# Performance work log

Measured on AMD Instinct MI355X. Metric: run time of the kernel, lower is better.

Reference implementation:

```python
import jax, jax.numpy as jnp
import numpy as np

N = 50000      # nodes
E = 800000     # edges (before self loops)
F_IN = 128     # dataset.num_features
HID = 32       # hidden_channels (per GAT head)
HEADS = 4
C = 40         # dataset.num_classes
NEG_SLOPE = 0.2


def setup_inputs() -> dict:
    key = jax.random.key(0)
    ks = jax.random.split(key, 18)
    g = lambda k, shape, fan: jax.random.normal(k, shape, dtype=jnp.float32) / np.sqrt(fan)
    inp = {
        "x": jax.random.normal(ks[0], (N, F_IN), dtype=jnp.float32),
        "edge_index": jax.random.randint(ks[1], (2, E), 0, N, dtype=jnp.int64),
        # GAT layer 1: F_IN -> HEADS*HID
        "gat_W1": g(ks[2], (F_IN, HEADS * HID), F_IN),
        "gat_att_src1": g(ks[3], (HEADS, HID), HID),
        "gat_att_dst1": g(ks[4], (HEADS, HID), HID),
        "gat_b1": jnp.zeros((HEADS * HID,), jnp.float32),
        # GAT layer 2: HEADS*HID -> C, heads=1
        "gat_W2": g(ks[5], (HEADS * HID, C), HEADS * HID),
        "gat_att_src2": g(ks[6], (1, C), C),
        "gat_att_dst2": g(ks[7], (1, C), C),
        "gat_b2": jnp.zeros((C,), jnp.float32),
        # GCN layers
        "gcn_W1": g(ks[8], (F_IN, HID), F_IN),
        "gcn_b1": jnp.zeros((HID,), jnp.float32),
        "gcn_W2": g(ks[9], (HID, C), HID),
        "gcn_b2": jnp.zeros((C,), jnp.float32),
        # final linear: 2C -> C
        "lin_W": g(ks[10], (2 * C, C), 2 * C),
        "lin_b": jnp.zeros((C,), jnp.float32),
        "weight_c": jnp.float32(0.5),
        "weight_t": jnp.float32(0.5),
    }
    return inp


def _add_self_loops(src, dst, n):
    loop = jnp.arange(n, dtype=src.dtype)
    return jnp.concatenate([src, loop]), jnp.concatenate([dst, loop])


def _gat_conv(x, src, dst, n, W, att_src, att_dst, b, heads, out_dim):
    # h: [n, heads, out_dim]
    h = (x @ W).reshape(n, heads, out_dim)
    a_s = jnp.einsum('nhd,hd->nh', h, att_src)   # source-side attention logit
    a_d = jnp.einsum('nhd,hd->nh', h, att_dst)   # target-side attention logit
    e = jax.nn.leaky_relu(a_s[src] + a_d[dst], NEG_SLOPE)  # [E', heads]
    # softmax over incoming edges of each target node (self loops guarantee >=1 edge)
    m = jax.ops.segment_max(e, dst, num_segments=n)
    ex = jnp.exp(e - m[dst])
    s = jax.ops.segment_sum(ex, dst, num_segments=n)
    alpha = ex / s[dst]                          # [E', heads]
    out = jax.ops.segment_sum(h[src] * alpha[..., None], dst, num_segments=n)
    return out.reshape(n, heads * out_dim) + b


def _gcn_conv(x, src, dst, n, W, b):
    h = x @ W
    deg = jax.ops.segment_sum(jnp.ones(src.shape, h.dtype), dst, num_segments=n)
    norm = jax.lax.rsqrt(deg)                    # deg >= 1 (self loops)
    coef = (norm[src] * norm[dst])[:, None]
    return jax.ops.segment_sum(h[src] * coef, dst, num_segments=n) + b


def reference(x, edge_index, gat_W1, gat_att_src1, gat_att_dst1, gat_b1,
              gat_W2, gat_att_src2, gat_att_dst2, gat_b2,
              gcn_W1, gcn_b1, gcn_W2, gcn_b2, lin_W, lin_b,
              weight_c, weight_t):
    n = x.shape[0]
    src, dst = _add_self_loops(edge_index[0], edge_index[1], n)
    # GAT branch (dropout is identity at inference)
    x_gat = _gat_conv(x, src, dst, n, gat_W1, gat_att_src1, gat_att_dst1,
                      gat_b1, HEADS, HID)
    x_gat = jax.nn.elu(x_gat)
    x_gat = _gat_conv(x_gat, src, dst, n, gat_W2, gat_att_src2, gat_att_dst2,
                      gat_b2, 1, C)
    # GCN branch
    x_gcn = jax.nn.relu(_gcn_conv(x, src, dst, n, gcn_W1, gcn_b1))
    x_gcn = _gcn_conv(x_gcn, src, dst, n, gcn_W2, gcn_b2)
    # weighted feature concat + linear head
    cat = jnp.concatenate([x_gcn * weight_c, x_gat * weight_t], axis=1)  # [n, 2C]
    return cat @ lin_W + lin_b
```

## Files before the change

### kernel.cpp

```cpp
#include <hip/hip_runtime.h>
#include <math.h>

#define F_IN   128
#define HIDC   32
#define NHEAD  4
#define CDIM   40
#define NEG_SLOPE 0.2f
#define BCAP   4096
#define OVCAP  16384
#define SCHUNK 4096

typedef __attribute__((ext_vector_type(8))) short bf16x8;
typedef __attribute__((ext_vector_type(4))) float f32x4;

__device__ __forceinline__ float leakyf(float x) { return x > 0.f ? x : NEG_SLOPE * x; }

__device__ __forceinline__ float sel4(float4 v, int h) {
    return (h == 0) ? v.x : (h == 1) ? v.y : (h == 2) ? v.z : v.w;
}
__device__ __forceinline__ unsigned pack2_bf16(float a, float b) {
    unsigned ua = __float_as_uint(a);
    unsigned ub = __float_as_uint(b);
    ua = (ua + 0x7FFFu + ((ua >> 16) & 1u)) >> 16;
    ub = (ub + 0x7FFFu + ((ub >> 16) & 1u)) >> 16;
    return ua | (ub << 16);
}
__device__ __forceinline__ float2 unpack2_bf16(unsigned p) {
    return make_float2(__uint_as_float(p << 16), __uint_as_float(p & 0xFFFF0000u));
}

__global__ void wb_prep_kernel(const float* __restrict__ Wg, const float* __restrict__ Wc,
                               uint4* __restrict__ wbf)
{
    int b = blockIdx.x;
    int lane = threadIdx.x;
    int nt = b >> 2, ks = b & 3;
    int c = nt * 16 + (lane & 15);
    int k0 = ks * 32 + (lane >> 4) * 8;
    unsigned u[4];
#pragma unroll
    for (int jj = 0; jj < 4; ++jj) {
        int k = k0 + 2 * jj;
        float a0 = (c < 128) ? Wg[(size_t)k * 128 + c] : Wc[(size_t)k * 32 + (c - 128)];
        float a1 = (c < 128) ? Wg[(size_t)(k + 1) * 128 + c] : Wc[(size_t)(k + 1) * 32 + (c - 128)];
        u[jj] = pack2_bf16(a0, a1);
    }
    wbf[(size_t)b * 64 + lane] = make_uint4(u[0], u[1], u[2], u[3]);
}

__global__ __launch_bounds__(256) void gemm1_mfma_kernel(
    const float* __restrict__ X, const uint4* __restrict__ wbf,
    const float* __restrict__ aw_s, const float* __restrict__ aw_d,
    unsigned* __restrict__ hb,
    float* __restrict__ as1, float* __restrict__ ad1, int n)
{
    __shared__ float Ct[64][164];
    __shared__ float sw[128], dw[128];
    const int tid = threadIdx.x;
    const int w = tid >> 6, lane = tid & 63;
    const int m = lane & 15, q = lane >> 4;
    const int node0 = blockIdx.x * 64;
    if (tid < 128) { sw[tid] = aw_s[tid]; dw[tid] = aw_d[tid]; }

    f32x4 acc[10];
#pragma unroll
    for (int t = 0; t < 10; ++t) acc[t] = (f32x4){0.f, 0.f, 0.f, 0.f};

    const int row = node0 + w * 16 + m;
    const bool rv = row < n;
#pragma unroll
    for (int ks = 0; ks < 4; ++ks) {
        uint4 pa = make_uint4(0u, 0u, 0u, 0u);
        if (rv) {
            const float* xr = X + (size_t)row * 128 + ks * 32 + q * 8;
            float4 a0 = *(const float4*)xr;
            float4 a1 = *(const float4*)(xr + 4);
            pa = make_uint4(pack2_bf16(a0.x, a0.y), pack2_bf16(a0.z, a0.w),
                            pack2_bf16(a1.x, a1.y), pack2_bf16(a1.z, a1.w));
        }
        bf16x8 af = *(bf16x8*)&pa;
#pragma unroll
        for (int nt = 0; nt < 10; ++nt) {
            uint4 pb = wbf[(size_t)(nt * 4 + ks) * 64 + lane];
            bf16x8 bfv = *(bf16x8*)&pb;
            acc[nt] = __builtin_amdgcn_mfma_f32_16x16x32_bf16(af, bfv, acc[nt], 0, 0, 0);
        }
    }
#pragma unroll
    for (int nt = 0; nt < 10; ++nt)
#pragma unroll
        for (int r = 0; r < 4; ++r)
            Ct[w * 16 + q * 4 + r][nt * 16 + m] = acc[nt][r];
    __syncthreads();

    for (int i = tid; i < 64 * 64; i += 256) {
        int nd = i >> 6, u = i & 63;
        int gn = node0 + nd;
        if (gn < n)
            hb[(size_t)gn * 80 + u] = pack2_bf16(Ct[nd][2 * u], Ct[nd][2 * u + 1]);
    }
    for (int i = tid; i < 64 * 16; i += 256) {
        int nd = i >> 4, u = i & 15;
        int gn = node0 + nd;
        if (gn < n)
            hb[(size_t)gn * 80 + 64 + u] = pack2_bf16(Ct[nd][128 + 2 * u], Ct[nd][128 + 2 * u + 1]);
    }
    {
        int nd = tid >> 2, h = tid & 3;
        int gn = node0 + nd;
        if (gn < n) {
            float s = 0.f, d = 0.f;
#pragma unroll
            for (int k = 0; k < HIDC; ++k) {
                float v = Ct[nd][h * HIDC + k];
                s = fmaf(v, sw[h * HIDC + k], s);
                d = fmaf(v, dw[h * HIDC + k], d);
            }
            as1[(size_t)gn * 4 + h] = s;
            ad1[(size_t)gn * 4 + h] = d;
        }
    }
}

template<int K, int OUTC, int BN, int BK, int OSTRIDE = OUTC>
__global__ __launch_bounds__((OUTC / 4) * (BN / 4)) void gemm_tile(
    const float* __restrict__ X, const float* __restrict__ W,
    const float* __restrict__ bias, float* __restrict__ Y, int n)
{
    constexpr int CG = OUTC / 4;
    constexpr int NG = BN / 4;
    constexpr int NT = CG * NG;
    __shared__ float Xs[BK][BN + 4];
    __shared__ float Ws[BK][OUTC];
    const int tid = threadIdx.x;
    const int cg = tid % CG, ng = tid / CG;
    const int node0 = blockIdx.x * BN;
    float acc[4][4] = {};

    for (int kb = 0; kb < K; kb += BK) {
        for (int idx = tid; idx < BN * (BK / 4); idx += NT) {
            int nd = idx / (BK / 4);
            int kq = idx % (BK / 4);
            int gnode = node0 + nd;
            float4 v = (gnode < n) ? *(const float4*)&X[(size_t)gnode * K + kb + kq * 4]
                                   : make_float4(0.f, 0.f, 0.f, 0.f);
            Xs[kq * 4 + 0][nd] = v.x;
            Xs[kq * 4 + 1][nd] = v.y;
            Xs[kq * 4 + 2][nd] = v.z;
            Xs[kq * 4 + 3][nd] = v.w;
        }
        for (int idx = tid; idx < BK * CG; idx += NT) {
            int kk = idx / CG;
            int cq = idx % CG;
            *(float4*)&Ws[kk][cq * 4] = *(const float4*)&W[(size_t)(kb + kk) * OUTC + cq * 4];
        }
        __syncthreads();
#pragma unroll
        for (int k = 0; k < BK; ++k) {
            float4 xv = *(const float4*)&Xs[k][ng * 4];
            float4 wv = *(const float4*)&Ws[k][cg * 4];
            float xa[4] = {xv.x, xv.y, xv.z, xv.w};
            float wa[4] = {wv.x, wv.y, wv.z, wv.w};
#pragma unroll
            for (int j = 0; j < 4; ++j)
#pragma unroll
                for (int c = 0; c < 4; ++c)
                    acc[j][c] = fmaf(xa[j], wa[c], acc[j][c]);
        }
        __syncthreads();
    }

    float4 bv = make_float4(0.f, 0.f, 0.f, 0.f);
    if (bias) bv = *(const float4*)&bias[cg * 4];
#pragma unroll
    for (int j = 0; j < 4; ++j) {
        int gnode = node0 + ng * 4 + j;
        if (gnode < n) {
            float4 o = make_float4(acc[j][0] + bv.x, acc[j][1] + bv.y,
                                   acc[j][2] + bv.z, acc[j][3] + bv.w);
            *(float4*)&Y[(size_t)gnode * OSTRIDE + cg * 4] = o;
        }
    }
}

template<int K, int OUTC, int BN, int BK, int OSTRIDE_U, int OFF_U>
__global__ __launch_bounds__((OUTC / 4) * (BN / 4)) void gemm_tile_bb(
    const unsigned* __restrict__ Xb, const float* __restrict__ W,
    unsigned* __restrict__ Yb, int n)
{
    constexpr int CG = OUTC / 4;
    constexpr int NG = BN / 4;
    constexpr int NT = CG * NG;
    __shared__ float Xs[BK][BN + 4];
    __shared__ float Ws[BK][OUTC];
    const int tid = threadIdx.x;
    const int cg = tid % CG, ng = tid / CG;
    const int node0 = blockIdx.x * BN;
    float acc[4][4] = {};

    for (int kb = 0; kb < K; kb += BK) {
        for (int idx = tid; idx < BN * (BK / 8); idx += NT) {
            int nd = idx / (BK / 8);
            int kq = idx % (BK / 8);
            int gnode = node0 + nd;
            uint4 v = (gnode < n) ? *(const uint4*)&Xb[(size_t)gnode * (K / 2) + kb / 2 + kq * 4]
                                  : make_uint4(0u, 0u, 0u, 0u);
            float2 a = unpack2_bf16(v.x), b = unpack2_bf16(v.y);
            float2 c = unpack2_bf16(v.z), d = unpack2_bf16(v.w);
            Xs[kq * 8 + 0][nd] = a.x; Xs[kq * 8 + 1][nd] = a.y;
            Xs[kq * 8 + 2][nd] = b.x; Xs[kq * 8 + 3][nd] = b.y;
            Xs[kq * 8 + 4][nd] = c.x; Xs[kq * 8 + 5][nd] = c.y;
            Xs[kq * 8 + 6][nd] = d.x; Xs[kq * 8 + 7][nd] = d.y;
        }
        for (int idx = tid; idx < BK * CG; idx += NT) {
            int kk = idx / CG;
            int cq = idx % CG;
            *(float4*)&Ws[kk][cq * 4] = *(const float4*)&W[(size_t)(kb + kk) * OUTC + cq * 4];
        }
        __syncthreads();
#pragma unroll
        for (int k = 0; k < BK; ++k) {
            float4 xv = *(const float4*)&Xs[k][ng * 4];
            float4 wv = *(const float4*)&Ws[k][cg * 4];
            float xa[4] = {xv.x, xv.y, xv.z, xv.w};
            float wa[4] = {wv.x, wv.y, wv.z, wv.w};
#pragma unroll
            for (int j = 0; j < 4; ++j)
#pragma unroll
                for (int c = 0; c < 4; ++c)
                    acc[j][c] = fmaf(xa[j], wa[c], acc[j][c]);
        }
        __syncthreads();
    }

#pragma unroll
    for (int j = 0; j < 4; ++j) {
        int gnode = node0 + ng * 4 + j;
        if (gnode < n) {
            uint2 pb = make_uint2(pack2_bf16(acc[j][0], acc[j][1]),
                                  pack2_bf16(acc[j][2], acc[j][3]));
            *(uint2*)&Yb[(size_t)gnode * OSTRIDE_U + OFF_U + cg * 2] = pb;
        }
    }
}

__global__ __launch_bounds__(320) void gemm2_gat_kernel(
    const unsigned* __restrict__ Xb, const float* __restrict__ W,
    const float* __restrict__ aw_s, const float* __restrict__ aw_d,
    unsigned* __restrict__ Yb, float* __restrict__ as2, float* __restrict__ ad2, int n)
{
    constexpr int K = 128, OUTC = 40, BN = 128, BK = 32;
    constexpr int CG = OUTC / 4, NT = 320;
    __shared__ float smem[32 * 132 + 32 * 40];
    float* Xs = smem;
    float* Ws = smem + 32 * 132;
    const int tid = threadIdx.x;
    const int cg = tid % CG, ng = tid / CG;
    const int node0 = blockIdx.x * BN;
    float acc[4][4] = {};

    for (int kb = 0; kb < K; kb += BK) {
        for (int idx = tid; idx < BN * (BK / 8); idx += NT) {
            int nd = idx / (BK / 8);
            int kq = idx % (BK / 8);
            int gnode = node0 + nd;
            uint4 v = (gnode < n) ? *(const uint4*)&Xb[(size_t)gnode * (K / 2) + kb / 2 + kq * 4]
                                  : make_uint4(0u, 0u, 0u, 0u);
            float2 a = unpack2_bf16(v.x), b = unpack2_bf16(v.y);
            float2 c = unpack2_bf16(v.z), d = unpack2_bf16(v.w);
            Xs[(kq * 8 + 0) * 132 + nd] = a.x; Xs[(kq * 8 + 1) * 132 + nd] = a.y;
            Xs[(kq * 8 + 2) * 132 + nd] = b.x; Xs[(kq * 8 + 3) * 132 + nd] = b.y;
            Xs[(kq * 8 + 4) * 132 + nd] = c.x; Xs[(kq * 8 + 5) * 132 + nd] = c.y;
            Xs[(kq * 8 + 6) * 132 + nd] = d.x; Xs[(kq * 8 + 7) * 132 + nd] = d.y;
        }
        for (int idx = tid; idx < BK * CG; idx += NT) {
            int kk = idx / CG;
            int cq = idx % CG;
            *(float4*)&Ws[kk * 40 + cq * 4] = *(const float4*)&W[(size_t)(kb + kk) * OUTC + cq * 4];
        }
        __syncthreads();
#pragma unroll
        for (int k = 0; k < BK; ++k) {
            float4 xv = *(const float4*)&Xs[k * 132 + ng * 4];
            float4 wv = *(const float4*)&Ws[k * 40 + cg * 4];
            float xa[4] = {xv.x, xv.y, xv.z, xv.w};
            float wa[4] = {wv.x, wv.y, wv.z, wv.w};
#pragma unroll
            for (int j = 0; j < 4; ++j)
#pragma unroll
                for (int c = 0; c < 4; ++c)
                    acc[j][c] = fmaf(xa[j], wa[c], acc[j][c]);
        }
        __syncthreads();
    }

    float* Ct  = smem;
    float* sww = smem + 128 * 41;
    float* dww = sww + 40;
#pragma unroll
    for (int j = 0; j < 4; ++j) {
        int gnode = node0 + ng * 4 + j;
        if (gnode < n) {
            uint2 pb = make_uint2(pack2_bf16(acc[j][0], acc[j][1]),
                                  pack2_bf16(acc[j][2], acc[j][3]));
            *(uint2*)&Yb[(size_t)gnode * 40 + cg * 2] = pb;
        }
#pragma unroll
        for (int c = 0; c < 4; ++c)
            Ct[(ng * 4 + j) * 41 + cg * 4 + c] = acc[j][c];
    }
    if (tid < 40) { sww[tid] = aw_s[tid]; dww[tid] = aw_d[tid]; }
    __syncthreads();
    if (tid < 128) {
        int gnode = node0 + tid;
        if (gnode < n) {
            float s = 0.f, d = 0.f;
#pragma unroll
            for (int c = 0; c < 40; ++c) {
                float v = Ct[tid * 41 + c];
                s = fmaf(v, sww[c], s);
                d = fmaf(v, dww[c], d);
            }
            as2[gnode] = s;
            ad2[gnode] = d;
        }
    }
}

__global__ __launch_bounds__(256) void bucket_scatter_kernel(
    const int* __restrict__ src, const int* __restrict__ dst,
    unsigned* __restrict__ bcnt, unsigned* __restrict__ bpair,
    unsigned* __restrict__ ovf_cnt, uint2* __restrict__ ovf, int e, int nbuck)
{
    __shared__ unsigned hist[512];
    __shared__ unsigned base[512];
    const int t = threadIdx.x;
    const int lo = blockIdx.x * SCHUNK;
    const int hi = min(lo + SCHUNK, e);
    for (int i = t; i < nbuck; i += 256) hist[i] = 0;
    __syncthreads();
    for (int i = lo + t; i < hi; i += 256)
        atomicAdd(&hist[((unsigned)dst[i]) >> 7], 1u);
    __syncthreads();
    for (int i = t; i < nbuck; i += 256) {
        unsigned c = hist[i];
        base[i] = c ? atomicAdd(&bcnt[i], c) : 0u;
        hist[i] = 0;
    }
    __syncthreads();
    for (int i = lo + t; i < hi; i += 256) {
        unsigned s = (unsigned)src[i], d = (unsigned)dst[i];
        unsigned b = d >> 7;
        unsigned pos = base[b] + atomicAdd(&hist[b], 1u);
        if (pos < BCAP) bpair[(size_t)b * BCAP + pos] = s | ((d & 127u) << 16);
        else {
            unsigned o = atomicAdd(ovf_cnt, 1u);
            if (o < OVCAP) ovf[o] = make_uint2(s, d);
        }
    }
}

__global__ __launch_bounds__(256) void bucket_count_kernel(
    const unsigned* __restrict__ bcnt, const unsigned* __restrict__ bpair,
    const unsigned* __restrict__ ovf_cnt, const uint2* __restrict__ ovf,
    unsigned* __restrict__ counts, int n)
{
    __shared__ unsigned lc[128];
    const int b = blockIdx.x, base = b << 7;
    if (threadIdx.x < 128) lc[threadIdx.x] = 0;
    __syncthreads();
    unsigned bc = bcnt[b];
    int cnt = (int)(bc < BCAP ? bc : BCAP);
    for (int k = threadIdx.x; k < cnt; k += 256)
        atomicAdd(&lc[bpair[(size_t)b * BCAP + k] >> 16], 1u);
    unsigned oc_u = *ovf_cnt;
    int oc = (int)(oc_u < OVCAP ? oc_u : OVCAP);
    for (int k = threadIdx.x; k < oc; k += 256) {
        uint2 pp = ovf[k];
        if ((int)(pp.y >> 7) == b) atomicAdd(&lc[pp.y & 127u], 1u);
    }
    __syncthreads();
    int i = base + threadIdx.x;
    if (threadIdx.x < 128 && i < n) counts[i] = lc[threadIdx.x];
}

__global__ __launch_bounds__(256) void scan_reduce_kernel(const unsigned* __restrict__ counts,
                                                          unsigned* __restrict__ partials, int n)
{
    __shared__ unsigned sm[256];
    int t = threadIdx.x;
    int i = blockIdx.x * 256 + t;
    unsigned v = (i < n) ? counts[i] : 0u;
    sm[t] = v;
    __syncthreads();
#pragma unroll
    for (int off = 128; off > 0; off >>= 1) {
        if (t < off) sm[t] += sm[t + off];
        __syncthreads();
    }
    if (t == 0) partials[blockIdx.x] = sm[0];
}

__global__ __launch_bounds__(256) void scan_partials_kernel(unsigned* __restrict__ partials,
                                                            unsigned* __restrict__ rs, int nb, int n)
{
    __shared__ unsigned sm[256];
    int t = threadIdx.x;
    unsigned v = (t < nb) ? partials[t] : 0u;
    sm[t] = v;
    __syncthreads();
#pragma unroll
    for (int off = 1; off < 256; off <<= 1) {
        unsigned u = (t >= off) ? sm[t - off] : 0u;
        __syncthreads();
        sm[t] += u;
        __syncthreads();
    }
    if (t < nb) partials[t] = sm[t] - v;
    if (t == 255) rs[n] = sm[255];
}

__global__ __launch_bounds__(256) void scan_write_kernel(const unsigned* __restrict__ counts,
                                                         const unsigned* __restrict__ partials,
                                                         unsigned* __restrict__ rs,
                                                         float* __restrict__ nrm, int n)
{
    __shared__ unsigned sm[256];
    int t = threadIdx.x;
    int i = blockIdx.x * 256 + t;
    unsigned c = (i < n) ? counts[i] : 0u;
    sm[t] = c;
    __syncthreads();
#pragma unroll
    for (int off = 1; off < 256; off <<= 1) {
        unsigned u = (t >= off) ? sm[t - off] : 0u;
        __syncthreads();
        sm[t] += u;
        __syncthreads();
    }
    if (i < n) {
        rs[i] = partials[blockIdx.x] + sm[t] - c;
        nrm[i] = rsqrtf((float)(c + 1u));
    }
}

__global__ __launch_bounds__(256) void bucket_place_kernel(
    const unsigned* __restrict__ bcnt, const unsigned* __restrict__ bpair,
    const unsigned* __restrict__ rs, unsigned* __restrict__ csr_src,
    unsigned* __restrict__ cursor, int n)
{
    __shared__ unsigned lc[128];
    __shared__ unsigned rbase[128];
    const int b = blockIdx.x, base = b << 7;
    if (threadIdx.x < 128) {
        lc[threadIdx.x] = 0;
        int i = base + threadIdx.x;
        rbase[threadIdx.x] = (i < n) ? rs[i] : 0u;
    }
    __syncthreads();
    unsigned bc = bcnt[b];
    int cnt = (int)(bc < BCAP ? bc : BCAP);
    for (int k = threadIdx.x; k < cnt; k += 256) {
        unsigned v = bpair[(size_t)b * BCAP + k];
        unsigned ld = v >> 16;
        unsigned r = atomicAdd(&lc[ld], 1u);
        csr_src[rbase[ld] + r] = v & 0xFFFFu;
    }
    __syncthreads();
    int i = base + threadIdx.x;
    if (threadIdx.x < 128 && i < n) cursor[i] = rbase[threadIdx.x] + lc[threadIdx.x];
}

__global__ void overflow_fill_kernel(const unsigned* __restrict__ ovf_cnt,
                                     const uint2* __restrict__ ovf,
                                     unsigned* __restrict__ cursor,
                                     unsigned* __restrict__ csr_src)
{
    unsigned oc_u = *ovf_cnt;
    int oc = (int)(oc_u < OVCAP ? oc_u : OVCAP);
    for (int k = threadIdx.x; k < oc; k += 256) {
        uint2 pp = ovf[k];
        unsigned pos = atomicAdd(&cursor[pp.y], 1u);
        csr_src[pos] = pp.x;
    }
}

__global__ __launch_bounds__(256) void agg1_fused_kernel(
    const unsigned* __restrict__ hb,
    const float* __restrict__ as1, const float* __restrict__ ad1,
    const float* __restrict__ nrm,
    const unsigned* __restrict__ rs, const unsigned* __restrict__ csr_src,
    const float* __restrict__ gat_b1, const float* __restrict__ gcn_b1,
    unsigned* __restrict__ xgb, unsigned* __restrict__ gaccb, int n)
{
    const int wid = threadIdx.x >> 6;
    const int lane = threadIdx.x & 63;
    const int i = blockIdx.x * 4 + wid;
    if (i >= n) return;
    const unsigned beg = rs[i];
    const int deg = (int)(rs[i + 1] - beg);
    const float4* as1v = (const float4*)as1;
    const uint4*  hv4  = (const uint4*)hb;

    const int e = lane >> 4, c = lane & 15;
    const int h = c >> 2;
    const bool gc = c < 4;

    const float4 dv = ((const float4*)ad1)[i];
    const float dvh = sel4(dv, h);
    const float ni  = nrm[i];

    unsigned pre = (lane < deg) ? csr_src[beg + lane] : (unsigned)i;

    const float4 av = as1v[i];
    const float eself = __expf(leakyf(sel4(av, h) + dvh));

    float acc[8], gacc[8];
#pragma unroll
    for (int t = 0; t < 8; ++t) { acc[t] = 0.f; gacc[t] = 0.f; }
    float sumw = 0.f;

    if (e == 0) {
        uint4 hv = hv4[(size_t)i * 20 + c];
        float2 p0 = unpack2_bf16(hv.x), p1 = unpack2_bf16(hv.y);
        float2 p2 = unpack2_bf16(hv.z), p3 = unpack2_bf16(hv.w);
        acc[0] = p0.x * eself; acc[1] = p0.y * eself;
        acc[2] = p1.x * eself; acc[3] = p1.y * eself;
        acc[4] = p2.x * eself; acc[5] = p2.y * eself;
        acc[6] = p3.x * eself; acc[7] = p3.y * eself;
        if (gc) {
            uint4 gv = hv4[(size_t)i * 20 + 16 + c];
            float w2s = ni * ni;
            float2 q0 = unpack2_bf16(gv.x), q1 = unpack2_bf16(gv.y);
            float2 q2 = unpack2_bf16(gv.z), q3 = unpack2_bf16(gv.w);
            gacc[0] = q0.x * w2s; gacc[1] = q0.y * w2s;
            gacc[2] = q1.x * w2s; gacc[3] = q1.y * w2s;
            gacc[4] = q2.x * w2s; gacc[5] = q2.y * w2s;
            gacc[6] = q3.x * w2s; gacc[7] = q3.y * w2s;
        }
    }

    const int dfast = deg < 64 ? deg : 64;
    const int steps = (dfast + 3) >> 2;

    float4 a_cur = make_float4(0.f, 0.f, 0.f, 0.f);
    uint4  h_cur = make_uint4(0u, 0u, 0u, 0u);
    uint4  g_cur = make_uint4(0u, 0u, 0u, 0u);
    float  nr_cur = 0.f;
    if (steps > 0) {
        unsigned s = __shfl(pre, e, 64);
        if (e >= deg) s = (unsigned)i;
        a_cur = as1v[s];
        h_cur = hv4[(size_t)s * 20 + c];
        if (gc) { g_cur = hv4[(size_t)s * 20 + 16 + c]; nr_cur = nrm[s]; }
    }
    for (int j = 0; j < steps; ++j) {
        float4 a_nxt = a_cur;
        uint4  h_nxt = h_cur, g_nxt = g_cur;
        float  nr_nxt = nr_cur;
        if (j + 1 < steps) {
            int idx = (j + 1) * 4 + e;
            unsigned s = __shfl(pre, idx, 64);
            if (idx >= deg) s = (unsigned)i;
            a_nxt = as1v[s];
            h_nxt = hv4[(size_t)s * 20 + c];
            if (gc) { g_nxt = hv4[(size_t)s * 20 + 16 + c]; nr_nxt = nrm[s]; }
        }
        const bool val = (j * 4 + e) < deg;
        float w = __expf(leakyf(sel4(a_cur, h) + dvh));
        w = val ? w : 0.f;
        sumw += w;
        {
            float2 p0 = unpack2_bf16(h_cur.x), p1 = unpack2_bf16(h_cur.y);
            float2 p2 = unpack2_bf16(h_cur.z), p3 = unpack2_bf16(h_cur.w);
            acc[0] = fmaf(p0.x, w, acc[0]); acc[1] = fmaf(p0.y, w, acc[1]);
            acc[2] = fmaf(p1.x, w, acc[2]); acc[3] = fmaf(p1.y, w, acc[3]);
            acc[4] = fmaf(p2.x, w, acc[4]); acc[5] = fmaf(p2.y, w, acc[5]);
            acc[6] = fmaf(p3.x, w, acc[6]); acc[7] = fmaf(p3.y, w, acc[7]);
        }
        if (gc) {
            float cw = val ? nr_cur * ni : 0.f;
            float2 q0 = unpack2_bf16(g_cur.x), q1 = unpack2_bf16(g_cur.y);
            float2 q2 = unpack2_bf16(g_cur.z), q3 = unpack2_bf16(g_cur.w);
            gacc[0] = fmaf(q0.x, cw, gacc[0]); gacc[1] = fmaf(q0.y, cw, gacc[1]);
            gacc[2] = fmaf(q1.x, cw, gacc[2]); gacc[3] = fmaf(q1.y, cw, gacc[3]);
            gacc[4] = fmaf(q2.x, cw, gacc[4]); gacc[5] = fmaf(q2.y, cw, gacc[5]);
            gacc[6] = fmaf(q3.x, cw, gacc[6]); gacc[7] = fmaf(q3.y, cw, gacc[7]);
        }
        a_cur = a_nxt; h_cur = h_nxt; g_cur = g_nxt; nr_cur = nr_nxt;
    }
    for (int j4 = 64; j4 < deg; j4 += 4) {
        int idx = j4 + e;
        bool val = idx < deg;
        unsigned s = val ? csr_src[beg + idx] : (unsigned)i;
        float4 a = as1v[s];
        float w = val ? __expf(leakyf(sel4(a, h) + dvh)) : 0.f;
        sumw += w;
        uint4 hv = hv4[(size_t)s * 20 + c];
        float2 p0 = unpack2_bf16(hv.x), p1 = unpack2_bf16(hv.y);
        float2 p2 = unpack2_bf16(hv.z), p3 = unpack2_bf16(hv.w);
        acc[0] = fmaf(p0.x, w, acc[0]); acc[1] = fmaf(p0.y, w, acc[1]);
        acc[2] = fmaf(p1.x, w, acc[2]); acc[3] = fmaf(p1.y, w, acc[3]);
        acc[4] = fmaf(p2.x, w, acc[4]); acc[5] = fmaf(p2.y, w, acc[5]);
        acc[6] = fmaf(p3.x, w, acc[6]); acc[7] = fmaf(p3.y, w, acc[7]);
        if (gc) {
            float cw = val ? nrm[s] * ni : 0.f;
            uint4 gv = hv4[(size_t)s * 20 + 16 + c];
            float2 q0 = unpack2_bf16(gv.x), q1 = unpack2_bf16(gv.y);
            float2 q2 = unpack2_bf16(gv.z), q3 = unpack2_bf16(gv.w);
            gacc[0] = fmaf(q0.x, cw, gacc[0]); gacc[1] = fmaf(q0.y, cw, gacc[1]);
            gacc[2] = fmaf(q1.x, cw, gacc[2]); gacc[3] = fmaf(q1.y, cw, gacc[3]);
            gacc[4] = fmaf(q2.x, cw, gacc[4]); gacc[5] = fmaf(q2.y, cw, gacc[5]);
            gacc[6] = fmaf(q3.x, cw, gacc[6]); gacc[7] = fmaf(q3.y, cw, gacc[7]);
        }
    }

#pragma unroll
    for (int t = 0; t < 8; ++t) {
        acc[t]  += __shfl_xor(acc[t], 16, 64);
        acc[t]  += __shfl_xor(acc[t], 32, 64);
        gacc[t] += __shfl_xor(gacc[t], 16, 64);
        gacc[t] += __shfl_xor(gacc[t], 32, 64);
    }
    sumw += __shfl_xor(sumw, 16, 64);
    sumw += __shfl_xor(sumw, 32, 64);
    const float ssh = sumw + eself;

    if (e == 0) {
        float inv = 1.f / ssh;
        float4 b0 = *(const float4*)&gat_b1[c * 8];
        float4 b1 = *(const float4*)&gat_b1[c * 8 + 4];
        float o[8] = {acc[0] * inv + b0.x, acc[1] * inv + b0.y,
                      acc[2] * inv + b0.z, acc[3] * inv + b0.w,
                      acc[4] * inv + b1.x, acc[5] * inv + b1.y,
                      acc[6] * inv + b1.z, acc[7] * inv + b1.w};
#pragma unroll
        for (int t = 0; t < 8; ++t) o[t] = o[t] > 0.f ? o[t] : __expf(o[t]) - 1.f;
        uint4 pv = make_uint4(pack2_bf16(o[0], o[1]), pack2_bf16(o[2], o[3]),
                              pack2_bf16(o[4], o[5]), pack2_bf16(o[6], o[7]));
        ((uint4*)xgb)[(size_t)i * 16 + c] = pv;
        if (gc) {
            float4 c0 = *(const float4*)&gcn_b1[c * 8];
            float4 c1 = *(const float4*)&gcn_b1[c * 8 + 4];
            float g[8] = {fmaxf(gacc[0] + c0.x, 0.f), fmaxf(gacc[1] + c0.y, 0.f),
                          fmaxf(gacc[2] + c0.z, 0.f), fmaxf(gacc[3] + c0.w, 0.f),
                          fmaxf(gacc[4] + c1.x, 0.f), fmaxf(gacc[5] + c1.y, 0.f),
                          fmaxf(gacc[6] + c1.z, 0.f), fmaxf(gacc[7] + c1.w, 0.f)};
            uint4 gv = make_uint4(pack2_bf16(g[0], g[1]), pack2_bf16(g[2], g[3]),
                                  pack2_bf16(g[4], g[5]), pack2_bf16(g[6], g[7]));
            ((uint4*)gaccb)[(size_t)i * 4 + c] = gv;
        }
    }
}

__global__ __launch_bounds__(256) void agg2_fused_kernel(
    const unsigned* __restrict__ hg_b, const float* __restrict__ as2,
    const float* __restrict__ ad2, const float* __restrict__ nrm,
    const unsigned* __restrict__ rs, const unsigned* __restrict__ csr_src,
    const float* __restrict__ gat_b2, const float* __restrict__ gcn_b2,
    const float* __restrict__ wc_p, const float* __restrict__ wt_p,
    float* __restrict__ cat, int n)
{
    const int wid = threadIdx.x >> 6;
    const int lane = threadIdx.x & 63;
    const int i = blockIdx.x * 4 + wid;
    if (i >= n) return;
    const unsigned beg = rs[i];
    const int deg = (int)(rs[i + 1] - beg);
    const int e = lane & 3, c = lane >> 2;
    const bool act = c < 10, isgat = c < 5;
    const float adv = ad2[i];
    const float ni = nrm[i];
    const uint4* hgv = (const uint4*)hg_b;

    unsigned pre = (lane < deg) ? csr_src[beg + lane] : (unsigned)i;
    const float eself = __expf(leakyf(as2[i] + adv));

    float acc[8];
#pragma unroll
    for (int t = 0; t < 8; ++t) acc[t] = 0.f;
    float sumw = 0.f;

    if (act && e == 0) {
        uint4 hv = hgv[(size_t)i * 10 + c];
        float sw = isgat ? eself : ni * ni;
        float2 p0 = unpack2_bf16(hv.x), p1 = unpack2_bf16(hv.y);
        float2 p2 = unpack2_bf16(hv.z), p3 = unpack2_bf16(hv.w);
        acc[0] = p0.x * sw; acc[1] = p0.y * sw;
        acc[2] = p1.x * sw; acc[3] = p1.y * sw;
        acc[4] = p2.x * sw; acc[5] = p2.y * sw;
        acc[6] = p3.x * sw; acc[7] = p3.y * sw;
    }

    const int dfast = deg < 64 ? deg : 64;
    const int steps = (dfast + 3) >> 2;

    float aw_cur = 0.f;
    uint4 h_cur = make_uint4(0u, 0u, 0u, 0u);
    if (steps > 0) {
        unsigned s = __shfl(pre, e, 64);
        if (e >= deg) s = (unsigned)i;
        if (act) { aw_cur = isgat ? as2[s] : nrm[s]; h_cur = hgv[(size_t)s * 10 + c]; }
    }
    for (int j = 0; j < steps; ++j) {
        float aw_nxt = aw_cur;
        uint4 h_nxt = h_cur;
        if (j + 1 < steps) {
            int idx = (j + 1) * 4 + e;
            unsigned s = __shfl(pre, idx, 64);
            if (idx >= deg) s = (unsigned)i;
            if (act) { aw_nxt = isgat ? as2[s] : nrm[s]; h_nxt = hgv[(size_t)s * 10 + c]; }
        }
        const bool val = (j * 4 + e) < deg;
        float w;
        if (isgat) {
            w = __expf(leakyf(aw_cur + adv));
            w = val ? w : 0.f;
            sumw += w;
        } else {
            w = val ? aw_cur * ni : 0.f;
        }
        if (act) {
            float2 p0 = unpack2_bf16(h_cur.x), p1 = unpack2_bf16(h_cur.y);
            float2 p2 = unpack2_bf16(h_cur.z), p3 = unpack2_bf16(h_cur.w);
            acc[0] = fmaf(p0.x, w, acc[0]); acc[1] = fmaf(p0.y, w, acc[1]);
            acc[2] = fmaf(p1.x, w, acc[2]); acc[3] = fmaf(p1.y, w, acc[3]);
            acc[4] = fmaf(p2.x, w, acc[4]); acc[5] = fmaf(p2.y, w, acc[5]);
            acc[6] = fmaf(p3.x, w, acc[6]); acc[7] = fmaf(p3.y, w, acc[7]);
        }
        aw_cur = aw_nxt; h_cur = h_nxt;
    }
    for (int j4 = 64; j4 < deg; j4 += 4) {
        int idx = j4 + e;
        bool val = idx < deg;
        unsigned s = val ? csr_src[beg + idx] : (unsigned)i;
        if (act) {
            float aw = isgat ? as2[s] : nrm[s];
            float w;
            if (isgat) {
                w = val ? __expf(leakyf(aw + adv)) : 0.f;
                sumw += w;
            } else {
                w = val ? aw * ni : 0.f;
            }
            uint4 hv = hgv[(size_t)s * 10 + c];
            float2 p0 = unpack2_bf16(hv.x), p1 = unpack2_bf16(hv.y);
            float2 p2 = unpack2_bf16(hv.z), p3 = unpack2_bf16(hv.w);
            acc[0] = fmaf(p0.x, w, acc[0]); acc[1] = fmaf(p0.y, w, acc[1]);
            acc[2] = fmaf(p1.x, w, acc[2]); acc[3] = fmaf(p1.y, w, acc[3]);
            acc[4] = fmaf(p2.x, w, acc[4]); acc[5] = fmaf(p2.y, w, acc[5]);
            acc[6] = fmaf(p3.x, w, acc[6]); acc[7] = fmaf(p3.y, w, acc[7]);
        }
    }

#pragma unroll
    for (int t = 0; t < 8; ++t) {
        acc[t] += __shfl_xor(acc[t], 1, 64);
        acc[t] += __shfl_xor(acc[t], 2, 64);
    }
    sumw += __shfl_xor(sumw, 1, 64);
    sumw += __shfl_xor(sumw, 2, 64);
    const float ssum = sumw + eself;

    if (act && e == 0) {
        if (isgat) {
            float inv = 1.f / ssum, wt = *wt_p;
            float4 b0 = *(const float4*)&gat_b2[c * 8];
            float4 b1 = *(const float4*)&gat_b2[c * 8 + 4];
            float4 o0 = make_float4((acc[0] * inv + b0.x) * wt, (acc[1] * inv + b0.y) * wt,
                                    (acc[2] * inv + b0.z) * wt, (acc[3] * inv + b0.w) * wt);
            float4 o1 = make_float4((acc[4] * inv + b1.x) * wt, (acc[5] * inv + b1.y) * wt,
                                    (acc[6] * inv + b1.z) * wt, (acc[7] * inv + b1.w) * wt);
            *(float4*)&cat[(size_t)i * 80 + 40 + c * 8]     = o0;
            *(float4*)&cat[(size_t)i * 80 + 40 + c * 8 + 4] = o1;
        } else {
            float wc = *wc_p;
            int g = c - 5;
            float4 b0 = *(const float4*)&gcn_b2[g * 8];
            float4 b1 = *(const float4*)&gcn_b2[g * 8 + 4];
            float4 o0 = make_float4((acc[0] + b0.x) * wc, (acc[1] + b0.y) * wc,
                                    (acc[2] + b0.z) * wc, (acc[3] + b0.w) * wc);
            float4 o1 = make_float4((acc[4] + b1.x) * wc, (acc[5] + b1.y) * wc,
                                    (acc[6] + b1.z) * wc, (acc[7] + b1.w) * wc);
            *(float4*)&cat[(size_t)i * 80 + g * 8]     = o0;
            *(float4*)&cat[(size_t)i * 80 + g * 8 + 4] = o1;
        }
    }
}

extern "C" void kernel_launch(void* const* d_in, const int* in_sizes, int n_in,
                              void* d_out, int out_size, void* d_ws, size_t ws_size,
                              hipStream_t stream)
{
    const float* x        = (const float*)d_in[0];
    const int*   eidx     = (const int*)d_in[1];
    const float* gat_W1   = (const float*)d_in[2];
    const float* att_s1   = (const float*)d_in[3];
    const float* att_d1   = (const float*)d_in[4];
    const float* gat_b1   = (const float*)d_in[5];
    const float* gat_W2   = (const float*)d_in[6];
    const float* att_s2   = (const float*)d_in[7];
    const float* att_d2   = (const float*)d_in[8];
    const float* gat_b2   = (const float*)d_in[9];
    const float* gcn_W1   = (const float*)d_in[10];
    const float* gcn_b1   = (const float*)d_in[11];
    const float* gcn_W2   = (const float*)d_in[12];
    const float* gcn_b2   = (const float*)d_in[13];
    const float* lin_W    = (const float*)d_in[14];
    const float* lin_b    = (const float*)d_in[15];
    const float* wc_p     = (const float*)d_in[16];
    const float* wt_p     = (const float*)d_in[17];

    const int n = in_sizes[0] / F_IN;
    const int e = in_sizes[1] / 2;
    const int* src = eidx;
    const int* dst = eidx + e;
    const int NBUCK = (n + 127) >> 7;

    char* p = (char*)d_ws;
    auto alloc = [&](size_t bytes) -> void* {
        void* r = (void*)p;
        p += (bytes + 255) & ~(size_t)255;
        return r;
    };
    unsigned* counts  = (unsigned*)alloc((size_t)n * 4);
    unsigned* rs      = (unsigned*)alloc((size_t)(n + 1) * 4);
    unsigned* cursor  = (unsigned*)alloc((size_t)n * 4);
    unsigned* partials= (unsigned*)alloc(256 * 4);
    unsigned* bcnt    = (unsigned*)alloc((size_t)(NBUCK + 1) * 4);
    unsigned* csr_src = (unsigned*)alloc((size_t)e * 4);
    uint4*    wbf     = (uint4*)alloc(40 * 64 * 16);
    float* nrm     = (float*)alloc((size_t)n * 4);
    float* as1     = (float*)alloc((size_t)n * 4 * 4);
    float* ad1     = (float*)alloc((size_t)n * 4 * 4);
    float* as2     = (float*)alloc((size_t)n * 4);
    float* ad2     = (float*)alloc((size_t)n * 4);
    float* cat     = (float*)alloc((size_t)n * 80 * 4);
    unsigned* hg_b = (unsigned*)alloc((size_t)n * 40 * 4);
    float* xg      = (float*)alloc((size_t)n * F_IN * 4);
    unsigned* gaccb= (unsigned*)alloc((size_t)n * 16 * 4);
    unsigned* bpair = (unsigned*)cat;
    uint2*    ovf   = (uint2*)(bpair + (size_t)NBUCK * BCAP);
    unsigned* hb    = (unsigned*)cat;
    unsigned* xgb   = (unsigned*)xg;
    unsigned* ovf_cnt = bcnt + NBUCK;

    const int NB = (n + 255) / 256;
    const int WB = (n + 3) / 4;
    const int SB = (e + SCHUNK - 1) / SCHUNK;

    hipMemsetAsync(bcnt, 0, (size_t)(NBUCK + 1) * 4, stream);
    bucket_scatter_kernel<<<SB, 256, 0, stream>>>(src, dst, bcnt, bpair, ovf_cnt, ovf, e, NBUCK);
    bucket_count_kernel<<<NBUCK, 256, 0, stream>>>(bcnt, bpair, ovf_cnt, ovf, counts, n);
    scan_reduce_kernel<<<NB, 256, 0, stream>>>(counts, partials, n);
    scan_partials_kernel<<<1, 256, 0, stream>>>(partials, rs, NB, n);
    scan_write_kernel<<<NB, 256, 0, stream>>>(counts, partials, rs, nrm, n);
    bucket_place_kernel<<<NBUCK, 256, 0, stream>>>(bcnt, bpair, rs, csr_src, cursor, n);
    overflow_fill_kernel<<<1, 256, 0, stream>>>(ovf_cnt, ovf, cursor, csr_src);

    wb_prep_kernel<<<40, 64, 0, stream>>>(gat_W1, gcn_W1, wbf);
    gemm1_mfma_kernel<<<(n + 63) / 64, 256, 0, stream>>>(x, wbf, att_s1, att_d1,
                                                         hb, as1, ad1, n);

    agg1_fused_kernel<<<WB, 256, 0, stream>>>(hb, as1, ad1, nrm, rs, csr_src,
                                              gat_b1, gcn_b1, xgb, gaccb, n);

    gemm_tile_bb<32, 40, 128, 32, 40, 20><<<(n + 127) / 128, 320, 0, stream>>>(gaccb, gcn_W2, hg_b, n);
    gemm2_gat_kernel<<<(n + 127) / 128, 320, 0, stream>>>(xgb, gat_W2, att_s2, att_d2,
                                                          hg_b, as2, ad2, n);

    agg2_fused_kernel<<<WB, 256, 0, stream>>>(hg_b, as2, ad2, nrm, rs, csr_src,
                                              gat_b2, gcn_b2, wc_p, wt_p, cat, n);

    gemm_tile<80, 40, 128, 40><<<(n + 127) / 128, 320, 0, stream>>>(cat, lin_W, lin_b, (float*)d_out, n);
}
```

Measured before the change: 306.0 us.

## Fuse final linear head into agg2 kernel and fold bucket-count memset into prep

Applies the final 80x40 linear layer inside the second aggregation kernel. Each wavefront broadcasts its concatenated features via shuffles and multiplies them against lin_W staged in shared memory, so the [n,80] cat buffer is never written or re-read and one GEMM launch is removed. The hipMemsetAsync of the bucket counters is replaced by zeroing inside wb_prep_kernel, which now runs first, saving one stream operation. In exchange every agg2 block reloads the 12.8KB weight matrix into LDS, and the per-node matvec adds 80 shuffles per wave.

```diff
diff --git a/kernel.cpp b/kernel.cpp
--- a/kernel.cpp
+++ b/kernel.cpp
@@ -30,10 +30,13 @@
 }
 
 __global__ void wb_prep_kernel(const float* __restrict__ Wg, const float* __restrict__ Wc,
-                               uint4* __restrict__ wbf)
+                               uint4* __restrict__ wbf, unsigned* __restrict__ bcnt,
+                               int nbuck1)
 {
     int b = blockIdx.x;
     int lane = threadIdx.x;
+    int gtid = b * 64 + lane;
+    if (gtid < nbuck1) bcnt[gtid] = 0u;
     int nt = b >> 2, ks = b & 3;
     int c = nt * 16 + (lane & 15);
     int k0 = ks * 32 + (lane >> 4) * 8;
@@ -118,67 +121,6 @@
             }
             as1[(size_t)gn * 4 + h] = s;
             ad1[(size_t)gn * 4 + h] = d;
-        }
-    }
-}
-
-template<int K, int OUTC, int BN, int BK, int OSTRIDE = OUTC>
-__global__ __launch_bounds__((OUTC / 4) * (BN / 4)) void gemm_tile(
-    const float* __restrict__ X, const float* __restrict__ W,
-    const float* __restrict__ bias, float* __restrict__ Y, int n)
-{
-    constexpr int CG = OUTC / 4;
-    constexpr int NG = BN / 4;
-    constexpr int NT = CG * NG;
-    __shared__ float Xs[BK][BN + 4];
-    __shared__ float Ws[BK][OUTC];
-    const int tid = threadIdx.x;
-    const int cg = tid % CG, ng = tid / CG;
-    const int node0 = blockIdx.x * BN;
-    float acc[4][4] = {};
-
-    for (int kb = 0; kb < K; kb += BK) {
-        for (int idx = tid; idx < BN * (BK / 4); idx += NT) {
-            int nd = idx / (BK / 4);
-            int kq = idx % (BK / 4);
-            int gnode = node0 + nd;
-            float4 v = (gnode < n) ? *(const float4*)&X[(size_t)gnode * K + kb + kq * 4]
-                                   : make_float4(0.f, 0.f, 0.f, 0.f);
-            Xs[kq * 4 + 0][nd] = v.x;
-            Xs[kq * 4 + 1][nd] = v.y;
-            Xs[kq * 4 + 2][nd] = v.z;
-            Xs[kq * 4 + 3][nd] = v.w;
-        }
-        for (int idx = tid; idx < BK * CG; idx += NT) {
-            int kk = idx / CG;
-            int cq = idx % CG;
-            *(float4*)&Ws[kk][cq * 4] = *(const float4*)&W[(size_t)(kb + kk) * OUTC + cq * 4];
-        }
-        __syncthreads();
-#pragma unroll
-        for (int k = 0; k < BK; ++k) {
-            float4 xv = *(const float4*)&Xs[k][ng * 4];
-            float4 wv = *(const float4*)&Ws[k][cg * 4];
-            float xa[4] = {xv.x, xv.y, xv.z, xv.w};
-            float wa[4] = {wv.x, wv.y, wv.z, wv.w};
-#pragma unroll
-            for (int j = 0; j < 4; ++j)
-#pragma unroll
-                for (int c = 0; c < 4; ++c)
-                    acc[j][c] = fmaf(xa[j], wa[c], acc[j][c]);
-        }
-        __syncthreads();
-    }
-
-    float4 bv = make_float4(0.f, 0.f, 0.f, 0.f);
-    if (bias) bv = *(const float4*)&bias[cg * 4];
-#pragma unroll
-    for (int j = 0; j < 4; ++j) {
-        int gnode = node0 + ng * 4 + j;
-        if (gnode < n) {
-            float4 o = make_float4(acc[j][0] + bv.x, acc[j][1] + bv.y,
-                                   acc[j][2] + bv.z, acc[j][3] + bv.w);
-            *(float4*)&Y[(size_t)gnode * OSTRIDE + cg * 4] = o;
         }
     }
 }
@@ -659,10 +601,19 @@
     const unsigned* __restrict__ rs, const unsigned* __restrict__ csr_src,
     const float* __restrict__ gat_b2, const float* __restrict__ gcn_b2,
     const float* __restrict__ wc_p, const float* __restrict__ wt_p,
-    float* __restrict__ cat, int n)
-{
-    const int wid = threadIdx.x >> 6;
-    const int lane = threadIdx.x & 63;
+    const float* __restrict__ lin_W, const float* __restrict__ lin_b,
+    float* __restrict__ Y, int n)
+{
+    __shared__ float Wk[80 * 41];
+    const int tid = threadIdx.x;
+    for (int idx = tid; idx < 3200; idx += 256) {
+        int k = idx / 40, oc = idx - k * 40;
+        Wk[k * 41 + oc] = lin_W[idx];
+    }
+    __syncthreads();
+
+    const int wid = tid >> 6;
+    const int lane = tid & 63;
     const int i = blockIdx.x * 4 + wid;
     if (i >= n) return;
     const unsigned beg = rs[i];
@@ -762,30 +713,37 @@
     sumw += __shfl_xor(sumw, 2, 64);
     const float ssum = sumw + eself;
 
-    if (act && e == 0) {
-        if (isgat) {
-            float inv = 1.f / ssum, wt = *wt_p;
-            float4 b0 = *(const float4*)&gat_b2[c * 8];
-            float4 b1 = *(const float4*)&gat_b2[c * 8 + 4];
-            float4 o0 = make_float4((acc[0] * inv + b0.x) * wt, (acc[1] * inv + b0.y) * wt,
-                                    (acc[2] * inv + b0.z) * wt, (acc[3] * inv + b0.w) * wt);
-            float4 o1 = make_float4((acc[4] * inv + b1.x) * wt, (acc[5] * inv + b1.y) * wt,
-                                    (acc[6] * inv + b1.z) * wt, (acc[7] * inv + b1.w) * wt);
-            *(float4*)&cat[(size_t)i * 80 + 40 + c * 8]     = o0;
-            *(float4*)&cat[(size_t)i * 80 + 40 + c * 8 + 4] = o1;
-        } else {
-            float wc = *wc_p;
-            int g = c - 5;
-            float4 b0 = *(const float4*)&gcn_b2[g * 8];
-            float4 b1 = *(const float4*)&gcn_b2[g * 8 + 4];
-            float4 o0 = make_float4((acc[0] + b0.x) * wc, (acc[1] + b0.y) * wc,
-                                    (acc[2] + b0.z) * wc, (acc[3] + b0.w) * wc);
-            float4 o1 = make_float4((acc[4] + b1.x) * wc, (acc[5] + b1.y) * wc,
-                                    (acc[6] + b1.z) * wc, (acc[7] + b1.w) * wc);
-            *(float4*)&cat[(size_t)i * 80 + g * 8]     = o0;
-            *(float4*)&cat[(size_t)i * 80 + g * 8 + 4] = o1;
-        }
-    }
+    float cv[8];
+#pragma unroll
+    for (int t = 0; t < 8; ++t) cv[t] = 0.f;
+    if (isgat) {
+        float inv = 1.f / ssum, wt = *wt_p;
+        float4 b0 = *(const float4*)&gat_b2[c * 8];
+        float4 b1 = *(const float4*)&gat_b2[c * 8 + 4];
+        float bb[8] = {b0.x, b0.y, b0.z, b0.w, b1.x, b1.y, b1.z, b1.w};
+#pragma unroll
+        for (int t = 0; t < 8; ++t) cv[t] = (acc[t] * inv + bb[t]) * wt;
+    } else if (act) {
+        float wc = *wc_p;
+        float4 b0 = *(const float4*)&gcn_b2[(c - 5) * 8];
+        float4 b1 = *(const float4*)&gcn_b2[(c - 5) * 8 + 4];
+        float bb[8] = {b0.x, b0.y, b0.z, b0.w, b1.x, b1.y, b1.z, b1.w};
+#pragma unroll
+        for (int t = 0; t < 8; ++t) cv[t] = (acc[t] + bb[t]) * wc;
+    }
+
+    const int oc = lane < 40 ? lane : 0;
+    float o = lin_b[oc];
+#pragma unroll
+    for (int kc = 0; kc < 10; ++kc) {
+        const int srcl = 4 * (kc < 5 ? 5 + kc : kc - 5);
+#pragma unroll
+        for (int t = 0; t < 8; ++t) {
+            float ca = __shfl(cv[t], srcl, 64);
+            o = fmaf(ca, Wk[(kc * 8 + t) * 41 + oc], o);
+        }
+    }
+    if (lane < 40) Y[(size_t)i * 40 + lane] = o;
 }
 
 extern "C" void kernel_launch(void* const* d_in, const int* in_sizes, int n_in,
@@ -835,13 +793,12 @@
     float* ad1     = (float*)alloc((size_t)n * 4 * 4);
     float* as2     = (float*)alloc((size_t)n * 4);
     float* ad2     = (float*)alloc((size_t)n * 4);
-    float* cat     = (float*)alloc((size_t)n * 80 * 4);
+    unsigned* hb   = (unsigned*)alloc((size_t)n * 80 * 4);
     unsigned* hg_b = (unsigned*)alloc((size_t)n * 40 * 4);
     float* xg      = (float*)alloc((size_t)n * F_IN * 4);
     unsigned* gaccb= (unsigned*)alloc((size_t)n * 16 * 4);
-    unsigned* bpair = (unsigned*)cat;
+    unsigned* bpair = hb;
     uint2*    ovf   = (uint2*)(bpair + (size_t)NBUCK * BCAP);
-    unsigned* hb    = (unsigned*)cat;
     unsigned* xgb   = (unsigned*)xg;
     unsigned* ovf_cnt = bcnt + NBUCK;
 
@@ -849,7 +806,8 @@
     const int WB = (n + 3) / 4;
     const int SB = (e + SCHUNK - 1) / SCHUNK;
 
-    hipMemsetAsync(bcnt, 0, (size_t)(NBUCK + 1) * 4, stream);
+    wb_prep_kernel<<<40, 64, 0, stream>>>(gat_W1, gcn_W1, wbf, bcnt, NBUCK + 1);
+
     bucket_scatter_kernel<<<SB, 256, 0, stream>>>(src, dst, bcnt, bpair, ovf_cnt, ovf, e, NBUCK);
     bucket_count_kernel<<<NBUCK, 256, 0, stream>>>(bcnt, bpair, ovf_cnt, ovf, counts, n);
     scan_reduce_kernel<<<NB, 256, 0, stream>>>(counts, partials, n);
@@ -858,7 +816,6 @@
     bucket_place_kernel<<<NBUCK, 256, 0, stream>>>(bcnt, bpair, rs, csr_src, cursor, n);
     overflow_fill_kernel<<<1, 256, 0, stream>>>(ovf_cnt, ovf, cursor, csr_src);
 
-    wb_prep_kernel<<<40, 64, 0, stream>>>(gat_W1, gcn_W1, wbf);
     gemm1_mfma_kernel<<<(n + 63) / 64, 256, 0, stream>>>(x, wbf, att_s1, att_d1,
                                                          hb, as1, ad1, n);
 
@@ -870,7 +827,6 @@
                                                           hg_b, as2, ad2, n);
 
     agg2_fused_kernel<<<WB, 256, 0, stream>>>(hg_b, as2, ad2, nrm, rs, csr_src,
-                                              gat_b2, gcn_b2, wc_p, wt_p, cat, n);
-
-    gemm_tile<80, 40, 128, 40><<<(n + 127) / 128, 320, 0, stream>>>(cat, lin_W, lin_b, (float*)d_out, n);
-}
+                                              gat_b2, gcn_b2, wc_p, wt_p,
+                                              lin_W, lin_b, (float*)d_out, n);
+}
```

Result: slower. 372.8 us (+21.8%).
